# Kernel optimization log

Hardware: AMD Instinct MI355X
Metric: run time of the kernel (lower is better)

The kernel has to match this reference:

```python
import jax, jax.numpy as jnp
import numpy as np

E = 1024      # embed_dim
H = 16        # num_heads
D = E // H    # head_dim = 64
K = 4         # num_hyper_nodes
MAX_SEQ = 8192
ROPE_BASE = 10000.0
SCALE = D ** -0.5


def rotate_half(x):
    half = x.shape[-1] // 2
    return jnp.concatenate([-x[..., half:], x[..., :half]], axis=-1)


def _rope_cache():
    inv_freq = 1.0 / (ROPE_BASE ** (jnp.arange(0, D, 2, dtype=jnp.float32) / D))
    t = jnp.arange(MAX_SEQ, dtype=jnp.float32)
    freqs = jnp.outer(t, inv_freq)                       # (MAX_SEQ, D/2)
    emb = jnp.concatenate([freqs, freqs], axis=-1)       # (MAX_SEQ, D)
    return jnp.cos(emb), jnp.sin(emb)


def setup_inputs() -> dict:
    key = jax.random.key(0)
    ks = jax.random.split(key, 6)
    B, S = 2, 2048
    w_scale = E ** -0.5  # keep pre-softmax logits in a sane range
    return {
        "x":  jax.random.normal(ks[0], (B, S, E), dtype=jnp.float32),
        "Wq": jax.random.normal(ks[1], (E, E), dtype=jnp.float32) * w_scale,
        "Wk": jax.random.normal(ks[2], (E, E), dtype=jnp.float32) * w_scale,
        "Wv": jax.random.normal(ks[3], (E, E), dtype=jnp.float32) * w_scale,
        "Wr": jax.random.normal(ks[4], (E, H * K), dtype=jnp.float32) * w_scale,
        "Wo": jax.random.normal(ks[5], (E, E), dtype=jnp.float32) * w_scale,
    }


def reference(x, Wq, Wk, Wv, Wr, Wo):
    B, S, _ = x.shape
    # projections -> (B, H, S, D)
    q = (x @ Wq).reshape(B, S, H, D).transpose(0, 2, 1, 3)
    k = (x @ Wk).reshape(B, S, H, D).transpose(0, 2, 1, 3)
    v = (x @ Wv).reshape(B, S, H, D).transpose(0, 2, 1, 3)

    # node routing probabilities (B, H, S, K)
    logits = (x @ Wr).reshape(B, S, H, K).transpose(0, 2, 1, 3)
    node_probs = jax.nn.softmax(logits, axis=-1)

    # expected per-node position: sum_{j<i} p[j,k]  -> (B, H, S, K)
    expected_pos = jnp.cumsum(node_probs, axis=2) - node_probs

    # fractional-position RoPE via linear interpolation of the cos/sin cache
    cos_c, sin_c = _rope_cache()
    pos = jnp.clip(expected_pos, 0.0, MAX_SEQ - 1)
    pf = pos.astype(jnp.int32)                   # floor
    pc = jnp.minimum(pf + 1, MAX_SEQ - 1)        # ceil
    frac = (pos - pf.astype(pos.dtype))[..., None]
    cos = cos_c[pf] + frac * (cos_c[pc] - cos_c[pf])   # (B,H,S,K,D)
    sin = sin_c[pf] + frac * (sin_c[pc] - sin_c[pf])

    # Weighted combine over nodes. Since q_k = q*cos_k + rh(q)*sin_k is linear
    # in (cos_k, sin_k), sum_k p_k * q_k = q * (sum_k p_k cos_k) + rh(q) * (sum_k p_k sin_k)
    cos_w = jnp.einsum('bhsk,bhskd->bhsd', node_probs, cos)
    sin_w = jnp.einsum('bhsk,bhskd->bhsd', node_probs, sin)
    q_r = q * cos_w + rotate_half(q) * sin_w
    k_r = k * cos_w + rotate_half(k) * sin_w

    # P(same node) weights (B, H, S, S)
    node_w = jnp.einsum('bhik,bhjk->bhij', node_probs, node_probs)

    scores = jnp.einsum('bhid,bhjd->bhij', q_r, k_r) * SCALE
    scores = scores + jnp.log(node_w + 1e-8)
    causal = jnp.tril(jnp.ones((S, S), dtype=bool))
    scores = jnp.where(causal[None, None], scores, -jnp.inf)
    attn = jax.nn.softmax(scores, axis=-1)

    out = jnp.einsum('bhij,bhjd->bhid', attn, v)
    out = out.transpose(0, 2, 1, 3).reshape(B, S, E)
    return out @ Wo
```

## Files before the change

kernel.cpp:

```cpp
#include <hip/hip_runtime.h>

#define E_ 1024
#define H_ 16
#define D_ 64
#define K_ 4
#define S_ 2048
#define B_ 2
#define BS_ 4096
#define BH_ 32
#define CT_ 2080

typedef __attribute__((ext_vector_type(8))) short short8;
typedef __attribute__((ext_vector_type(4))) float f32x4;
typedef __attribute__((ext_vector_type(4))) unsigned short u16x4;

__device__ __forceinline__ unsigned short f2bf(float f) {
  union { float f; unsigned u; } v; v.f = f;
  unsigned r = v.u + 0x7FFFu + ((v.u >> 16) & 1u);
  return (unsigned short)(r >> 16);
}
__device__ __forceinline__ float bf2f(unsigned short u) {
  union { unsigned u; float f; } v; v.u = ((unsigned)u) << 16; return v.f;
}

typedef __attribute__((address_space(1))) const void gvoid;
typedef __attribute__((address_space(3))) void lvoid;
__device__ __forceinline__ void gload_lds16(const void* g, void* l) {
  __builtin_amdgcn_global_load_lds((gvoid*)g, (lvoid*)l, 16, 0, 0);
}

__device__ __forceinline__ short8 lds8(const unsigned short* base, int row, int chunk) {
  int off = row * 128 + (((chunk ^ (row & 7)) & 7) << 4);
  return *(const short8*)((const char*)base + off);
}

__device__ __forceinline__ float redmax16(float v) {
  int iv = __float_as_int(v);
  v = fmaxf(v, __int_as_float(__builtin_amdgcn_update_dpp(iv, iv, 0xB1, 0xF, 0xF, true)));
  iv = __float_as_int(v);
  v = fmaxf(v, __int_as_float(__builtin_amdgcn_update_dpp(iv, iv, 0x4E, 0xF, 0xF, true)));
  v = fmaxf(v, __shfl_xor(v, 4, 16));
  v = fmaxf(v, __shfl_xor(v, 8, 16));
  return v;
}

__global__ __launch_bounds__(256) void k_convert_x(const float* __restrict__ x,
                                                   unsigned short* __restrict__ xb) {
  int i = blockIdx.x * 256 + threadIdx.x;
  float4 v = ((const float4*)x)[i];
  u16x4 o; o.x = f2bf(v.x); o.y = f2bf(v.y); o.z = f2bf(v.z); o.w = f2bf(v.w);
  ((u16x4*)xb)[i] = o;
}

__global__ __launch_bounds__(256) void k_transpose_w(const float* __restrict__ Wq,
    const float* __restrict__ Wk, const float* __restrict__ Wv, const float* __restrict__ Wo,
    unsigned short* __restrict__ wt) {
  const float* W = blockIdx.z == 0 ? Wq : blockIdx.z == 1 ? Wk : blockIdx.z == 2 ? Wv : Wo;
  unsigned short* out = wt + (size_t)blockIdx.z * E_ * E_;
  __shared__ float tile[64][65];
  int k0 = blockIdx.y * 64, n0 = blockIdx.x * 64;
  int r = threadIdx.x >> 2, q4 = threadIdx.x & 3;
#pragma unroll
  for (int q = 0; q < 4; q++) {
    int c4 = q4 + q * 4;
    float4 v = *(const float4*)&W[(size_t)(k0 + r) * E_ + n0 + c4 * 4];
    tile[r][c4 * 4 + 0] = v.x; tile[r][c4 * 4 + 1] = v.y;
    tile[r][c4 * 4 + 2] = v.z; tile[r][c4 * 4 + 3] = v.w;
  }
  __syncthreads();
#pragma unroll
  for (int q = 0; q < 4; q++) {
    int cb = (q4 + q * 4) * 4;
    u16x4 o;
    o.x = f2bf(tile[cb + 0][r]); o.y = f2bf(tile[cb + 1][r]);
    o.z = f2bf(tile[cb + 2][r]); o.w = f2bf(tile[cb + 3][r]);
    *(u16x4*)&out[(size_t)(n0 + r) * E_ + k0 + cb] = o;
  }
}

__global__ __launch_bounds__(256) void k_cache(float* __restrict__ cosc, float* __restrict__ sinc) {
  int i = blockIdx.x * 256 + threadIdx.x;
  if (i >= CT_ * 32) return;
  int tt = i >> 5, f = i & 31;
  float invf = __expf(-(float)(2 * f) * (9.210340371976184f / 64.f));
  float ang = (float)tt * invf;
  cosc[i] = cosf(ang); sinc[i] = sinf(ang);
}

__global__ __launch_bounds__(256) void k_router(const float* __restrict__ x,
    const float* __restrict__ Wr, float* __restrict__ logits) {
  int rowblk = blockIdx.x * 8;
  int c = threadIdx.x & 63, rg = threadIdx.x >> 6;
  __shared__ float xs[8][128];
  float acc0 = 0.f, acc1 = 0.f;
  for (int e0 = 0; e0 < E_; e0 += 128) {
    __syncthreads();
    int idx = threadIdx.x;
    float4 v = *(const float4*)&x[(size_t)(rowblk + (idx >> 5)) * E_ + e0 + (idx & 31) * 4];
    *(float4*)&xs[idx >> 5][(idx & 31) * 4] = v;
    __syncthreads();
#pragma unroll 8
    for (int e = 0; e < 128; e++) {
      float w = Wr[(size_t)(e0 + e) * 64 + c];
      acc0 = fmaf(xs[rg * 2 + 0][e], w, acc0);
      acc1 = fmaf(xs[rg * 2 + 1][e], w, acc1);
    }
  }
  logits[(size_t)(rowblk + rg * 2 + 0) * 64 + c] = acc0;
  logits[(size_t)(rowblk + rg * 2 + 1) * 64 + c] = acc1;
}

__global__ __launch_bounds__(256) void k_scan(const float* __restrict__ logits,
    float* __restrict__ probs, unsigned short* __restrict__ pb, float* __restrict__ epos) {
  int bh = blockIdx.x; int b = bh >> 4, h = bh & 15;
  int t = threadIdx.x;
  float p[8][4];
  float own[4] = {0.f, 0.f, 0.f, 0.f};
#pragma unroll
  for (int r = 0; r < 8; r++) {
    int s = t * 8 + r;
    float4 lg = *(const float4*)&logits[(size_t)(b * S_ + s) * 64 + h * 4];
    float m = fmaxf(fmaxf(lg.x, lg.y), fmaxf(lg.z, lg.w));
    float e0 = __expf(lg.x - m), e1 = __expf(lg.y - m), e2 = __expf(lg.z - m), e3 = __expf(lg.w - m);
    float inv = 1.f / (e0 + e1 + e2 + e3);
    p[r][0] = e0 * inv; p[r][1] = e1 * inv; p[r][2] = e2 * inv; p[r][3] = e3 * inv;
    own[0] += p[r][0]; own[1] += p[r][1]; own[2] += p[r][2]; own[3] += p[r][3];
    float4 pv; pv.x = p[r][0]; pv.y = p[r][1]; pv.z = p[r][2]; pv.w = p[r][3];
    *(float4*)&probs[((size_t)bh * S_ + s) * 4] = pv;
    u16x4 pu; pu.x = f2bf(p[r][0]); pu.y = f2bf(p[r][1]);
    pu.z = f2bf(p[r][2]); pu.w = f2bf(p[r][3]);
    *(u16x4*)&pb[((size_t)bh * S_ + s) * 4] = pu;
  }
  __shared__ float sc[4][256];
#pragma unroll
  for (int k = 0; k < 4; k++) sc[k][t] = own[k];
  __syncthreads();
  for (int off = 1; off < 256; off <<= 1) {
    float v0 = 0, v1 = 0, v2 = 0, v3 = 0;
    if (t >= off) { v0 = sc[0][t - off]; v1 = sc[1][t - off]; v2 = sc[2][t - off]; v3 = sc[3][t - off]; }
    __syncthreads();
    if (t >= off) { sc[0][t] += v0; sc[1][t] += v1; sc[2][t] += v2; sc[3][t] += v3; }
    __syncthreads();
  }
  float run[4];
#pragma unroll
  for (int k = 0; k < 4; k++) run[k] = sc[k][t] - own[k];
#pragma unroll
  for (int r = 0; r < 8; r++) {
    int s = t * 8 + r;
    float4 ev; ev.x = run[0]; ev.y = run[1]; ev.z = run[2]; ev.w = run[3];
    *(float4*)&epos[((size_t)bh * S_ + s) * 4] = ev;
    run[0] += p[r][0]; run[1] += p[r][1]; run[2] += p[r][2]; run[3] += p[r][3];
  }
}

__global__ __launch_bounds__(256) void k_cwsw(const float* __restrict__ probs,
    const float* __restrict__ epos, const float* __restrict__ cosc, const float* __restrict__ sinc,
    float* __restrict__ cw, float* __restrict__ sw) {
  int bh = blockIdx.y;
  int s = blockIdx.x * 8 + (threadIdx.x >> 5);
  int f = threadIdx.x & 31;
  size_t row = (size_t)bh * S_ + s;
  float cacc = 0.f, sacc = 0.f;
#pragma unroll
  for (int k = 0; k < 4; k++) {
    float pk = probs[row * 4 + k];
    float pos = epos[row * 4 + k];
    pos = fminf(fmaxf(pos, 0.f), (float)(CT_ - 2));
    int pf = (int)pos; float fr = pos - (float)pf;
    float c0 = cosc[pf * 32 + f], c1 = cosc[pf * 32 + 32 + f];
    float s0 = sinc[pf * 32 + f], s1 = sinc[pf * 32 + 32 + f];
    cacc = fmaf(pk, c0 + fr * (c1 - c0), cacc);
    sacc = fmaf(pk, s0 + fr * (s1 - s0), sacc);
  }
  cw[row * 32 + f] = cacc; sw[row * 32 + f] = sacc;
}

__device__ __forceinline__ void gemm_128x128(const unsigned short* __restrict__ A,
    const unsigned short* __restrict__ Bt, int m0, int n0,
    unsigned short* lA, unsigned short* lB, f32x4 acc[4][4]) {
  int t = threadIdx.x, w = t >> 6, lane = t & 63;
  int wm = w >> 1, wn = w & 1;
  int arow = lane & 15, agrp = lane >> 4;
  for (int k0 = 0; k0 < E_; k0 += 64) {
    __syncthreads();
#pragma unroll
    for (int j = 0; j < 4; j++) {
      int c = j * 256 + w * 64 + lane;
      int row = c >> 3, slot = c & 7;
      gload_lds16(A + (size_t)(m0 + row) * E_ + k0 + ((slot ^ (row & 7)) << 3),
                  lA + (size_t)(j * 256 + w * 64) * 8);
      gload_lds16(Bt + (size_t)(n0 + row) * E_ + k0 + ((slot ^ (row & 7)) << 3),
                  lB + (size_t)(j * 256 + w * 64) * 8);
    }
    __syncthreads();
#pragma unroll
    for (int ks = 0; ks < 2; ks++) {
      short8 af[4], bfr[4];
#pragma unroll
      for (int mi = 0; mi < 4; mi++) af[mi] = lds8(lA, wm * 64 + mi * 16 + arow, ks * 4 + agrp);
#pragma unroll
      for (int nj = 0; nj < 4; nj++) bfr[nj] = lds8(lB, wn * 64 + nj * 16 + arow, ks * 4 + agrp);
#pragma unroll
      for (int mi = 0; mi < 4; mi++)
#pragma unroll
        for (int nj = 0; nj < 4; nj++)
          acc[mi][nj] = __builtin_amdgcn_mfma_f32_16x16x32_bf16(af[mi], bfr[nj], acc[mi][nj], 0, 0, 0);
    }
  }
}

__global__ __launch_bounds__(256) void k_gemm_qkv(const unsigned short* __restrict__ xb,
    const unsigned short* __restrict__ wt, const float* __restrict__ cw, const float* __restrict__ sw,
    unsigned short* __restrict__ qr, unsigned short* __restrict__ kr, unsigned short* __restrict__ vb) {
  __shared__ unsigned short lA[128 * 64], lB[128 * 64];
  int z = blockIdx.z;
  int m0 = blockIdx.y * 128, n0 = blockIdx.x * 128;
  f32x4 acc[4][4];
  f32x4 zero4 = {0.f, 0.f, 0.f, 0.f};
#pragma unroll
  for (int a = 0; a < 4; a++)
#pragma unroll
    for (int b2 = 0; b2 < 4; b2++) acc[a][b2] = zero4;
  gemm_128x128(xb, wt + (size_t)z * E_ * E_, m0, n0, lA, lB, acc);

  int t = threadIdx.x, w = t >> 6, lane = t & 63;
  int wm = w >> 1, wn = w & 1;
  int arow = lane & 15, agrp = lane >> 4;
  if (z == 2) {
#pragma unroll
    for (int mi = 0; mi < 4; mi++) {
      int i0 = m0 + wm * 64 + mi * 16 + agrp * 4;
      int b = i0 >> 11, s0 = i0 & 2047;
#pragma unroll
      for (int nj = 0; nj < 4; nj++) {
        int col = n0 + wn * 64 + nj * 16 + arow;
        int h = col >> 6, dl = col & 63;
        u16x4 o;
        o.x = f2bf(acc[mi][nj][0]); o.y = f2bf(acc[mi][nj][1]);
        o.z = f2bf(acc[mi][nj][2]); o.w = f2bf(acc[mi][nj][3]);
        *(u16x4*)&vb[((size_t)(b * H_ + h) * 64 + dl) * S_ + s0] = o;
      }
    }
  } else {
    unsigned short* out = (z == 0) ? qr : kr;
    float scl = (z == 0) ? 0.18033688011f : 1.0f;
    int h = (n0 + wn * 64) >> 6;
#pragma unroll
    for (int mi = 0; mi < 4; mi++)
#pragma unroll
      for (int reg = 0; reg < 4; reg++) {
        int i = m0 + wm * 64 + mi * 16 + agrp * 4 + reg;
        int b = i >> 11, s = i & 2047;
        size_t rbase = (size_t)(b * H_ + h) * S_ + s;
        float cw0 = cw[rbase * 32 + arow], cw1 = cw[rbase * 32 + 16 + arow];
        float sw0 = sw[rbase * 32 + arow], sw1 = sw[rbase * 32 + 16 + arow];
#pragma unroll
        for (int nj = 0; nj < 4; nj++) {
          float v = acc[mi][nj][reg];
          float part = acc[mi][nj ^ 2][reg];
          float rh = (nj < 2) ? -part : part;
          float cwv = (nj & 1) ? cw1 : cw0;
          float swv = (nj & 1) ? sw1 : sw0;
          out[rbase * 64 + nj * 16 + arow] = f2bf((v * cwv + rh * swv) * scl);
        }
      }
  }
}

__global__ __launch_bounds__(256) void k_gemm_out(const unsigned short* __restrict__ ob,
    const unsigned short* __restrict__ wot, float* __restrict__ dout) {
  __shared__ unsigned short lA[64 * 64];
  __shared__ unsigned short lB[128 * 64];
  int m0 = blockIdx.y * 64, n0 = blockIdx.x * 128;
  int t = threadIdx.x, w = t >> 6, lane = t & 63;
  int arow = lane & 15, agrp = lane >> 4;
  f32x4 acc[4][2];
  f32x4 zero4 = {0.f, 0.f, 0.f, 0.f};
#pragma unroll
  for (int a = 0; a < 4; a++) { acc[a][0] = zero4; acc[a][1] = zero4; }
  for (int k0 = 0; k0 < E_; k0 += 64) {
    __syncthreads();
#pragma unroll
    for (int j = 0; j < 2; j++) {
      int c = j * 256 + t;
      int row = c >> 3, slot = c & 7;
      gload_lds16(ob + (size_t)(m0 + row) * E_ + k0 + ((slot ^ (row & 7)) << 3),
                  lA + (size_t)c * 8);
    }
#pragma unroll
    for (int j = 0; j < 4; j++) {
      int c = j * 256 + t;
      int row = c >> 3, slot = c & 7;
      gload_lds16(wot + (size_t)(n0 + row) * E_ + k0 + ((slot ^ (row & 7)) << 3),
                  lB + (size_t)c * 8);
    }
    __syncthreads();
#pragma unroll
    for (int ks = 0; ks < 2; ks++) {
      short8 af[4], bfr[2];
#pragma unroll
      for (int mi = 0; mi < 4; mi++) af[mi] = lds8(lA, mi * 16 + arow, ks * 4 + agrp);
#pragma unroll
      for (int nj = 0; nj < 2; nj++) bfr[nj] = lds8(lB, w * 32 + nj * 16 + arow, ks * 4 + agrp);
#pragma unroll
      for (int mi = 0; mi < 4; mi++)
#pragma unroll
        for (int nj = 0; nj < 2; nj++)
          acc[mi][nj] = __builtin_amdgcn_mfma_f32_16x16x32_bf16(af[mi], bfr[nj], acc[mi][nj], 0, 0, 0);
    }
  }
#pragma unroll
  for (int mi = 0; mi < 4; mi++)
#pragma unroll
    for (int reg = 0; reg < 4; reg++) {
      int i = m0 + mi * 16 + agrp * 4 + reg;
#pragma unroll
      for (int nj = 0; nj < 2; nj++) {
        int col = n0 + w * 32 + nj * 16 + arow;
        dout[(size_t)i * E_ + col] = acc[mi][nj][reg];
      }
    }
}

__device__ const int4 kChunk[38] = {
  { 8,0, 8, 8},{ 8,9,17, 9},{12,0, 8,19},{12,9,17,20},
  { 7,0, 7, 6},{ 7,8,15, 7},{10,0, 7,13},{11,0, 7,16},{11,8,15,17},{11,16,23,18},
  {12,18,25,21},{14,0, 7,26},{14,8,15,27},{15,0, 7,30},{15,8,15,31},{15,16,23,32},
  {15,24,31,33},{ 3,0, 7,-1},
  { 6,0, 6, 4},{ 6,7,13, 5},{ 9,0, 6,10},{ 9,7,13,11},{10,8,14,14},{10,15,21,15},
  {13,0, 6,22},{13,7,13,23},{13,14,20,24},{13,21,27,25},{14,16,22,28},{14,23,29,29},
  { 5,0, 5, 2},{ 5,6,11, 3},{ 9,14,19,12},{ 2,0, 5,-1},
  { 4,0, 4, 0},{ 4,5, 9, 1},{ 1,0, 3,-1},{ 0,0, 1,-1}
};

__device__ __forceinline__ void qk_phase(const unsigned short* lKc, const short8 qf[2][2],
                                         int arow, int agrp, f32x4 sacc[2][4]) {
#pragma unroll
  for (int ks = 0; ks < 2; ks++)
#pragma unroll
    for (int ct = 0; ct < 4; ct++) {
      short8 kf = lds8(lKc, ct * 16 + arow, ks * 4 + agrp);
      sacc[0][ct] = __builtin_amdgcn_mfma_f32_16x16x32_bf16(qf[0][ks], kf, sacc[0][ct], 0, 0, 0);
      sacc[1][ct] = __builtin_amdgcn_mfma_f32_16x16x32_bf16(qf[1][ks], kf, sacc[1][ct], 0, 0, 0);
    }
}

__device__ __forceinline__ void softmax_half(const f32x4 sacc[4], const short8 piF,
    const short8 pjF[4], unsigned short* lPh, int kv0, int ig_base, int arow, int agrp,
    float mrow[4], f32x4 oacc[4], f32x4& o4) {
  f32x4 eps4 = {1e-8f, 1e-8f, 1e-8f, 1e-8f};
  f32x4 nwa[4];
#pragma unroll
  for (int ct = 0; ct < 4; ct++)
    nwa[ct] = __builtin_amdgcn_mfma_f32_16x16x32_bf16(piF, pjF[ct], eps4, 0, 0, 0);
  float sv[4][4];
  float rmax[4] = {-1e30f, -1e30f, -1e30f, -1e30f};
  if (kv0 + 63 > ig_base) {
#pragma unroll
    for (int ct = 0; ct < 4; ct++) {
      int jg = kv0 + ct * 16 + arow;
#pragma unroll
      for (int reg = 0; reg < 4; reg++) {
        int ig = ig_base + agrp * 4 + reg;
        float xv = sacc[ct][reg];
        if (jg > ig) xv = -1e30f;
        sv[ct][reg] = xv;
        rmax[reg] = fmaxf(rmax[reg], xv);
      }
    }
  } else {
#pragma unroll
    for (int ct = 0; ct < 4; ct++)
#pragma unroll
      for (int reg = 0; reg < 4; reg++) {
        float xv = sacc[ct][reg];
        sv[ct][reg] = xv;
        rmax[reg] = fmaxf(rmax[reg], xv);
      }
  }
#pragma unroll
  for (int reg = 0; reg < 4; reg++) rmax[reg] = redmax16(rmax[reg]);
  bool ok = (rmax[0] <= mrow[0] + 11.5f) & (rmax[1] <= mrow[1] + 11.5f) &
            (rmax[2] <= mrow[2] + 11.5f) & (rmax[3] <= mrow[3] + 11.5f);
  if (!__all(ok)) {
    float alpha[4];
#pragma unroll
    for (int reg = 0; reg < 4; reg++) {
      float mn = fmaxf(mrow[reg], rmax[reg]);
      alpha[reg] = __builtin_amdgcn_exp2f(mrow[reg] - mn);
      mrow[reg] = mn;
    }
#pragma unroll
    for (int dt = 0; dt < 4; dt++) {
      f32x4 o = oacc[dt];
      o.x *= alpha[0]; o.y *= alpha[1]; o.z *= alpha[2]; o.w *= alpha[3];
      oacc[dt] = o;
    }
    o4.x *= alpha[0]; o4.y *= alpha[1]; o4.z *= alpha[2]; o4.w *= alpha[3];
  }
#pragma unroll
  for (int ct = 0; ct < 4; ct++)
#pragma unroll
    for (int reg = 0; reg < 4; reg++)
      sv[ct][reg] = __builtin_amdgcn_exp2f(sv[ct][reg] - mrow[reg]) * nwa[ct][reg];
#pragma unroll
  for (int ct = 0; ct < 4; ct++) {
    int col2 = (ct * 16 + arow) * 2;
#pragma unroll
    for (int rp = 0; rp < 2; rp++) {
      unsigned pk;
      asm("v_cvt_pk_bf16_f32 %0, %1, %2" : "=v"(pk) : "v"(sv[ct][rp * 2]), "v"(sv[ct][rp * 2 + 1]));
      int r0 = agrp * 4 + rp * 2, r1 = r0 + 1;
      *(unsigned short*)((char*)lPh + r0 * 128 + (col2 ^ ((r0 & 7) << 4))) = (unsigned short)pk;
      *(unsigned short*)((char*)lPh + r1 * 128 + (col2 ^ ((r1 & 7) << 4))) = (unsigned short)(pk >> 16);
    }
  }
}

__device__ __forceinline__ void pv_phase(const unsigned short* lP0, const unsigned short* lP1,
    const unsigned short* lVc, int arow, int agrp, f32x4 oacc0[4], f32x4 oacc1[4],
    f32x4& o40, f32x4& o41) {
  const short8 ones = {16256, 16256, 16256, 16256, 16256, 16256, 16256, 16256};
#pragma unroll
  for (int ks = 0; ks < 2; ks++) {
    short8 pf0 = lds8(lP0, arow, ks * 4 + agrp);
    short8 pf1 = lds8(lP1, arow, ks * 4 + agrp);
    o40 = __builtin_amdgcn_mfma_f32_16x16x32_bf16(pf0, ones, o40, 0, 0, 0);
    o41 = __builtin_amdgcn_mfma_f32_16x16x32_bf16(pf1, ones, o41, 0, 0, 0);
#pragma unroll
    for (int dt = 0; dt < 4; dt++) {
      short8 vf = lds8(lVc, dt * 16 + arow, ks * 4 + agrp);
      oacc0[dt] = __builtin_amdgcn_mfma_f32_16x16x32_bf16(pf0, vf, oacc0[dt], 0, 0, 0);
      oacc1[dt] = __builtin_amdgcn_mfma_f32_16x16x32_bf16(pf1, vf, oacc1[dt], 0, 0, 0);
    }
  }
}

__global__ __launch_bounds__(256, 2) void k_attn(const unsigned short* __restrict__ qr,
    const unsigned short* __restrict__ kr, const unsigned short* __restrict__ vb,
    const unsigned short* __restrict__ pb, unsigned short* __restrict__ ob,
    unsigned short* __restrict__ ObP, float* __restrict__ ml) {
  __shared__ unsigned short lK[2][64 * 64];
  __shared__ unsigned short lV[2][64 * 64];
  __shared__ unsigned short lP[4][2][16 * 64];
  int id = blockIdx.x;
  int xcd = id & 7, slt = id >> 3;
  int bh = xcd * 4 + (slt & 3);
  int4 ck = kChunk[slt >> 2];
  int qt2 = ck.x, j0 = ck.y, j1 = ck.z, part = ck.w;
  int t = threadIdx.x, w = t >> 6, lane = t & 63;
  int arow = lane & 15, agrp = lane >> 4;
  int q0 = qt2 * 128;
  size_t base = (size_t)bh * S_ * 64;
  size_t bhS = (size_t)bh * S_;

  short8 qf[2][2];
  short8 piF[2];
  float mrow[2][4];
  f32x4 oacc[2][4];
  f32x4 o4[2];
  f32x4 zero4 = {0.f, 0.f, 0.f, 0.f};
#pragma unroll
  for (int hh = 0; hh < 2; hh++) {
#pragma unroll
    for (int ks = 0; ks < 2; ks++)
      qf[hh][ks] = *(const short8*)&qr[base + (size_t)(q0 + hh * 64 + w * 16 + arow) * 64 + ks * 32 + agrp * 8];
    u16x4 pv = {0, 0, 0, 0};
    if (agrp == 0) pv = *(const u16x4*)&pb[(bhS + q0 + hh * 64 + w * 16 + arow) * 4];
    short8 z = {0, 0, 0, 0, 0, 0, 0, 0};
    z[0] = (short)pv.x; z[1] = (short)pv.y; z[2] = (short)pv.z; z[3] = (short)pv.w;
    piF[hh] = z;
#pragma unroll
    for (int reg = 0; reg < 4; reg++) mrow[hh][reg] = -1e30f;
#pragma unroll
    for (int dt = 0; dt < 4; dt++) oacc[hh][dt] = zero4;
    o4[hh] = zero4;
  }

  auto stageK = [&](int jt, int buf) {
#pragma unroll
    for (int j = 0; j < 2; j++) {
      int c = j * 256 + w * 64 + lane;
      int row = c >> 3, slot = c & 7;
      gload_lds16(kr + base + (size_t)(jt * 64 + row) * 64 + ((slot ^ (row & 7)) << 3),
                  &lK[buf][(size_t)(j * 256 + w * 64) * 8]);
    }
  };
  auto stageV = [&](int jt, int buf) {
#pragma unroll
    for (int j = 0; j < 2; j++) {
      int c = j * 256 + w * 64 + lane;
      int row = c >> 3, slot = c & 7;
      gload_lds16(vb + base + (size_t)row * S_ + jt * 64 + ((slot ^ (row & 7)) << 3),
                  &lV[buf][(size_t)(j * 256 + w * 64) * 8]);
    }
  };
  auto loadPj = [&](int jt, u16x4 pj[4]) {
#pragma unroll
    for (int ct = 0; ct < 4; ct++) {
      u16x4 z = {0, 0, 0, 0};
      if (agrp == 0) z = *(const u16x4*)&pb[(bhS + jt * 64 + ct * 16 + arow) * 4];
      pj[ct] = z;
    }
  };

  u16x4 pjv[4], pjvn[4];
  stageK(j0, 0);
  stageV(j0, 0);
  loadPj(j0, pjv);
  __syncthreads();

  int nt = j1 - j0 + 1;
  for (int i = 0; i < nt; i++) {
    int cur = i & 1;
    int kv0 = (j0 + i) * 64;
    bool hn = (i + 1) < nt;
    if (hn) {
      stageK(j0 + i + 1, cur ^ 1);
      stageV(j0 + i + 1, cur ^ 1);
    }

    f32x4 sacc[2][4];
#pragma unroll
    for (int hh = 0; hh < 2; hh++)
#pragma unroll
      for (int ct = 0; ct < 4; ct++) sacc[hh][ct] = zero4;

    __builtin_amdgcn_s_setprio(1);
    qk_phase(&lK[cur][0], qf, arow, agrp, sacc);
    __builtin_amdgcn_s_setprio(0);

    short8 pjF[4];
#pragma unroll
    for (int ct = 0; ct < 4; ct++) {
      short8 z = {0, 0, 0, 0, 0, 0, 0, 0};
      z[0] = (short)pjv[ct].x; z[1] = (short)pjv[ct].y;
      z[2] = (short)pjv[ct].z; z[3] = (short)pjv[ct].w;
      pjF[ct] = z;
    }
#pragma unroll
    for (int hh = 0; hh < 2; hh++)
      softmax_half(sacc[hh], piF[hh], pjF, &lP[w][hh][0], kv0, q0 + hh * 64 + w * 16,
                   arow, agrp, mrow[hh], oacc[hh], o4[hh]);

    if (hn) loadPj(j0 + i + 1, pjvn);

    asm volatile("s_waitcnt lgkmcnt(0)" ::: "memory");
    __builtin_amdgcn_sched_barrier(0);
    __builtin_amdgcn_s_setprio(1);
    pv_phase(&lP[w][0][0], &lP[w][1][0], &lV[cur][0], arow, agrp, oacc[0], oacc[1],
             o4[0], o4[1]);
    __builtin_amdgcn_s_setprio(0);
    if (hn) {
#pragma unroll
      for (int ct = 0; ct < 4; ct++) pjv[ct] = pjvn[ct];
    }
    __syncthreads();
  }

  if (part >= 0) {
    unsigned short* Op = ObP + ((size_t)bh * 34 + part) * 8192;
    float* mlp = ml + ((size_t)bh * 34 + part) * 256;
#pragma unroll
    for (int hh = 0; hh < 2; hh++) {
#pragma unroll
      for (int dt = 0; dt < 4; dt++)
#pragma unroll
        for (int reg = 0; reg < 4; reg++) {
          int row = hh * 64 + w * 16 + agrp * 4 + reg;
          Op[row * 64 + dt * 16 + arow] = f2bf(oacc[hh][dt][reg]);
        }
      if (arow == 0) {
#pragma unroll
        for (int reg = 0; reg < 4; reg++) {
          int row = hh * 64 + w * 16 + agrp * 4 + reg;
          mlp[row] = mrow[hh][reg];
          mlp[128 + row] = o4[hh][reg];
        }
      }
    }
  } else {
    int b = bh >> 4, h8 = bh & 15;
#pragma unroll
    for (int hh = 0; hh < 2; hh++) {
      f32x4 inv4;
      inv4.x = 1.f / o4[hh].x; inv4.y = 1.f / o4[hh].y;
      inv4.z = 1.f / o4[hh].z; inv4.w = 1.f / o4[hh].w;
#pragma unroll
      for (int dt = 0; dt < 4; dt++)
#pragma unroll
        for (int reg = 0; reg < 4; reg++) {
          int i = q0 + hh * 64 + w * 16 + agrp * 4 + reg;
          int d = dt * 16 + arow;
          float v = oacc[hh][dt][reg] * inv4[reg];
          ob[((size_t)(b * S_ + i) * H_ + h8) * 64 + d] = f2bf(v);
        }
    }
  }
}

__global__ __launch_bounds__(256) void k_merge(const unsigned short* __restrict__ ObP,
    const float* __restrict__ ml, unsigned short* __restrict__ ob) {
  int qx = blockIdx.x, bh = blockIdx.y;
  int qt2 = 4 + qx;
  int np = qt2 <= 8 ? 2 : (qt2 <= 12 ? 3 : 4);
  int bslot = qt2 <= 8 ? (qt2 - 4) * 2 : (qt2 <= 12 ? 10 + (qt2 - 9) * 3 : 22 + (qt2 - 13) * 4);
  int t = threadIdx.x;
  int r = t >> 1, dh = (t & 1) * 32;
  float mp[4], lp[4];
  float m = -1e30f;
  for (int p2 = 0; p2 < np; p2++) {
    const float* mlp = ml + ((size_t)bh * 34 + bslot + p2) * 256;
    mp[p2] = mlp[r]; lp[p2] = mlp[128 + r];
    m = fmaxf(m, mp[p2]);
  }
  float a[4], l = 0.f;
  for (int p2 = 0; p2 < np; p2++) { a[p2] = __builtin_amdgcn_exp2f(mp[p2] - m); l = fmaf(lp[p2], a[p2], l); }
  float inv = 1.f / l;
  for (int p2 = 0; p2 < np; p2++) a[p2] *= inv;
  int i = qt2 * 128 + r, b = bh >> 4, h = bh & 15;
  unsigned short* op = ob + ((size_t)(b * S_ + i) * H_ + h) * 64 + dh;
#pragma unroll
  for (int q = 0; q < 8; q++) {
    float a0 = 0.f, a1 = 0.f, a2 = 0.f, a3 = 0.f;
    for (int p2 = 0; p2 < np; p2++) {
      const unsigned short* Op = ObP + ((size_t)bh * 34 + bslot + p2) * 8192 + r * 64 + dh + q * 4;
      u16x4 xx = *(const u16x4*)Op;
      a0 = fmaf(bf2f(xx.x), a[p2], a0);
      a1 = fmaf(bf2f(xx.y), a[p2], a1);
      a2 = fmaf(bf2f(xx.z), a[p2], a2);
      a3 = fmaf(bf2f(xx.w), a[p2], a3);
    }
    u16x4 o; o.x = f2bf(a0); o.y = f2bf(a1); o.z = f2bf(a2); o.w = f2bf(a3);
    *(u16x4*)(op + q * 4) = o;
  }
}

extern "C" void kernel_launch(void* const* d_in, const int* in_sizes, int n_in,
                              void* d_out, int out_size, void* d_ws, size_t ws_size,
                              hipStream_t stream) {
  const float* x  = (const float*)d_in[0];
  const float* Wq = (const float*)d_in[1];
  const float* Wk = (const float*)d_in[2];
  const float* Wv = (const float*)d_in[3];
  const float* Wr = (const float*)d_in[4];
  const float* Wo = (const float*)d_in[5];
  float* dout = (float*)d_out;

  char* p = (char*)d_ws;
  auto alloc = [&](size_t bytes) -> char* {
    char* r = p; p += (bytes + 255) & ~(size_t)255; return r;
  };
  unsigned short* xb   = (unsigned short*)alloc((size_t)BS_ * E_ * 2);
  unsigned short* wt   = (unsigned short*)alloc((size_t)4 * E_ * E_ * 2);
  float* cosc          = (float*)alloc((size_t)CT_ * 32 * 4);
  float* sinc          = (float*)alloc((size_t)CT_ * 32 * 4);
  float* probs         = (float*)alloc((size_t)BH_ * S_ * 4 * 4);
  unsigned short* pb   = (unsigned short*)alloc((size_t)BH_ * S_ * 4 * 2);
  float* logits        = (float*)alloc((size_t)BS_ * 64 * 4);
  float* epos          = (float*)alloc((size_t)BH_ * S_ * 4 * 4);
  float* cw            = (float*)alloc((size_t)BH_ * S_ * 32 * 4);
  float* sw            = (float*)alloc((size_t)BH_ * S_ * 32 * 4);
  unsigned short* qrb  = (unsigned short*)alloc((size_t)BH_ * S_ * 64 * 2);
  unsigned short* krb  = (unsigned short*)alloc((size_t)BH_ * S_ * 64 * 2);
  unsigned short* vbb  = (unsigned short*)alloc((size_t)BH_ * S_ * 64 * 2);
  unsigned short* obb  = (unsigned short*)alloc((size_t)BS_ * E_ * 2);
  if ((size_t)(p - (char*)d_ws) > ws_size) return;

  unsigned short* ObP = (unsigned short*)logits;
  float* mlbuf = (float*)xb;

  k_convert_x<<<BS_ * E_ / 4 / 256, 256, 0, stream>>>(x, xb);
  k_transpose_w<<<dim3(16, 16, 4), 256, 0, stream>>>(Wq, Wk, Wv, Wo, wt);
  k_cache<<<(CT_ * 32 + 255) / 256, 256, 0, stream>>>(cosc, sinc);
  k_router<<<BS_ / 8, 256, 0, stream>>>(x, Wr, logits);
  k_scan<<<BH_, 256, 0, stream>>>(logits, probs, pb, epos);
  k_cwsw<<<dim3(S_ / 8, BH_), 256, 0, stream>>>(probs, epos, cosc, sinc, cw, sw);
  k_gemm_qkv<<<dim3(8, 32, 3), 256, 0, stream>>>(xb, wt, cw, sw, qrb, krb, vbb);
  k_attn<<<dim3(38 * BH_), 256, 0, stream>>>(qrb, krb, vbb, pb, obb, ObP, mlbuf);
  k_merge<<<dim3(12, BH_), 256, 0, stream>>>(ObP, mlbuf, obb);
  k_gemm_out<<<dim3(8, 64), 256, 0, stream>>>(obb, wt + (size_t)3 * E_ * E_, dout);
}
```

Before: 208.7 us.

## Restructure router GEMM with double-buffered LDS staging and 16-row register tiles

Rewrites the router projection kernel so each block computes 16 rows by 64 columns, staging both x and Wr chunks into double-buffered shared memory through direct global-to-LDS loads. Each thread accumulates a 1x4 output tile, reading vectorised values from a swizzled layout. The goal is to replace the per-element global Wr reads with shared-memory reuse and to overlap loading the next chunk with compute. It halves the grid size and depends on the gload_lds16 helper and the swizzle being correct.

```diff
diff --git a/kernel.cpp b/kernel.cpp
--- a/kernel.cpp
+++ b/kernel.cpp
@@ -89,25 +89,45 @@
 
 __global__ __launch_bounds__(256) void k_router(const float* __restrict__ x,
     const float* __restrict__ Wr, float* __restrict__ logits) {
-  int rowblk = blockIdx.x * 8;
-  int c = threadIdx.x & 63, rg = threadIdx.x >> 6;
-  __shared__ float xs[8][128];
-  float acc0 = 0.f, acc1 = 0.f;
-  for (int e0 = 0; e0 < E_; e0 += 128) {
+  __shared__ float xs[2][16 * 16 * 4];
+  __shared__ float ws[2][64 * 16 * 4];
+  int t = threadIdx.x;
+  int m0 = blockIdx.x * 16;
+  int r = t >> 4, cq = t & 15;
+  f32x4 acc = {0.f, 0.f, 0.f, 0.f};
+
+  auto stage = [&](int chunk, int buf) {
+    int e0 = chunk * 64;
+    gload_lds16(x + (size_t)(m0 + (t >> 4)) * E_ + e0 + (((t & 15) ^ (t >> 4)) << 2),
+                &xs[buf][(size_t)t * 4]);
+#pragma unroll
+    for (int j = 0; j < 4; j++) {
+      int slot = j * 256 + t;
+      gload_lds16(Wr + (size_t)(e0 + (slot >> 4)) * 64 + ((slot & 15) << 2),
+                  &ws[buf][(size_t)slot * 4]);
+    }
+  };
+
+  stage(0, 0);
+  __syncthreads();
+  for (int chunk = 0; chunk < 16; chunk++) {
+    int cur = chunk & 1;
+    if (chunk < 15) stage(chunk + 1, cur ^ 1);
+#pragma unroll
+    for (int e4 = 0; e4 < 16; e4++) {
+      f32x4 xf = *(const f32x4*)&xs[cur][(r * 16 + (e4 ^ r)) * 4];
+#pragma unroll
+      for (int i = 0; i < 4; i++) {
+        f32x4 wf = *(const f32x4*)&ws[cur][((e4 * 4 + i) * 16 + cq) * 4];
+        acc[0] = fmaf(xf[i], wf[0], acc[0]);
+        acc[1] = fmaf(xf[i], wf[1], acc[1]);
+        acc[2] = fmaf(xf[i], wf[2], acc[2]);
+        acc[3] = fmaf(xf[i], wf[3], acc[3]);
+      }
+    }
     __syncthreads();
-    int idx = threadIdx.x;
-    float4 v = *(const float4*)&x[(size_t)(rowblk + (idx >> 5)) * E_ + e0 + (idx & 31) * 4];
-    *(float4*)&xs[idx >> 5][(idx & 31) * 4] = v;
-    __syncthreads();
-#pragma unroll 8
-    for (int e = 0; e < 128; e++) {
-      float w = Wr[(size_t)(e0 + e) * 64 + c];
-      acc0 = fmaf(xs[rg * 2 + 0][e], w, acc0);
-      acc1 = fmaf(xs[rg * 2 + 1][e], w, acc1);
-    }
-  }
-  logits[(size_t)(rowblk + rg * 2 + 0) * 64 + c] = acc0;
-  logits[(size_t)(rowblk + rg * 2 + 1) * 64 + c] = acc1;
+  }
+  *(f32x4*)&logits[(size_t)(m0 + r) * 64 + cq * 4] = acc;
 }
 
 __global__ __launch_bounds__(256) void k_scan(const float* __restrict__ logits,
@@ -674,7 +694,7 @@
   k_convert_x<<<BS_ * E_ / 4 / 256, 256, 0, stream>>>(x, xb);
   k_transpose_w<<<dim3(16, 16, 4), 256, 0, stream>>>(Wq, Wk, Wv, Wo, wt);
   k_cache<<<(CT_ * 32 + 255) / 256, 256, 0, stream>>>(cosc, sinc);
-  k_router<<<BS_ / 8, 256, 0, stream>>>(x, Wr, logits);
+  k_router<<<BS_ / 16, 256, 0, stream>>>(x, Wr, logits);
   k_scan<<<BH_, 256, 0, stream>>>(logits, probs, pb, epos);
   k_cwsw<<<dim3(S_ / 8, BH_), 256, 0, stream>>>(probs, epos, cosc, sinc, cw, sw);
   k_gemm_qkv<<<dim3(8, 32, 3), 256, 0, stream>>>(xb, wt, cw, sw, qrb, krb, vbb);
```

New measurement: 192.4 us. 1.08x faster.
